# Kernel tuning notes

Hardware: AMD Instinct MI355X
Metric: run time of the kernel (lower is better)

The kernel has to match this reference:

```python
import jax, jax.numpy as jnp
import numpy as np

NUM_USERS = 50000
NUM_ITEMS = 40000
EMB = 64
NNZ = 2_000_000
BATCH = 1024


def setup_inputs() -> dict:
    key = jax.random.key(0)
    ks = jax.random.split(key, 10)
    graph_rows = jax.random.randint(ks[0], (NNZ,), 0, NUM_USERS, dtype=jnp.int32)
    graph_cols = jax.random.randint(ks[1], (NNZ,), 0, NUM_ITEMS, dtype=jnp.int32)
    graph_vals = jax.random.uniform(ks[2], (NNZ,), dtype=jnp.float32)
    Wq = jax.random.normal(ks[3], (2 * EMB, NUM_ITEMS), dtype=jnp.float32) * 0.01
    bq = jnp.zeros((2 * EMB,), jnp.float32)
    Wp = jax.random.normal(ks[4], (NUM_ITEMS, EMB), dtype=jnp.float32) * 0.01
    bp = jnp.zeros((NUM_ITEMS,), jnp.float32)
    user = jax.random.randint(ks[5], (BATCH,), 0, NUM_USERS, dtype=jnp.int32)
    x = (jax.random.uniform(ks[6], (BATCH, NUM_ITEMS)) < 0.02).astype(jnp.float32)
    eps = jax.random.normal(ks[7], (NUM_USERS, EMB), dtype=jnp.float32)
    return dict(graph_vals=graph_vals, Wq=Wq, bq=bq, Wp=Wp, bp=bp, x=x,
                eps=eps, graph_rows=graph_rows, graph_cols=graph_cols, user=user)


def reference(graph_vals, Wq, bq, Wp, bp, x, eps, graph_rows, graph_cols, user):
    # ---- encode: single SpMM  h = Graph @ Wq^T + bq   (dropout off / eval mode)
    # gather item rows of Wq^T per nonzero, scale, scatter-add into users
    gathered = graph_vals[:, None] * Wq.T[graph_cols]          # [nnz, 2E]
    h = jax.ops.segment_sum(gathered, graph_rows, num_segments=NUM_USERS) + bq  # [U, 2E]
    mu, logvar = h[:, :EMB], h[:, EMB:]                        # [U, E] each
    # ---- reparameterize: z = mu + eps * exp(0.5*logvar)
    z = mu + eps * jnp.exp(0.5 * logvar)
    # ---- decode batch users: single Linear(E -> I)
    zb = z[user]                                               # [B, E]
    recon = zb @ Wp.T + bp                                     # [B, I]
    # ---- Mult-VAE ELBO (anneal = 1.0)
    log_sm = jax.nn.log_softmax(recon, axis=-1)
    recon_loss = -jnp.mean(jnp.sum(log_sm * x, axis=-1))
    mu_b, lv_b = mu[user], logvar[user]
    kl_loss = -0.5 * jnp.mean(jnp.sum(1.0 + lv_b - mu_b * mu_b - jnp.exp(lv_b), axis=-1))
    return jnp.stack([recon_loss, kl_loss])  # [2]: (recon_loss, KL_loss)
```

## Files before the change

### kernel.cpp

```cpp
#include <hip/hip_runtime.h>
#include <cstdint>

#define NUM_USERS 50000
#define NUM_ITEMS 40000
#define EMB 64
#define NNZ_E 2000000
#define BATCH 1024
#define NCHB 125
#define SLOT_CAP 128
#define INF_I 0x7fffffff

typedef __attribute__((ext_vector_type(8))) short short8;
typedef __attribute__((ext_vector_type(4))) float float4v;

__device__ __forceinline__ unsigned short f2bf(float f) {
    union { float f; unsigned u; } x; x.f = f;
    unsigned r = x.u + 0x7fffu + ((x.u >> 16) & 1u);
    return (unsigned short)(r >> 16);
}
__device__ __forceinline__ float bf2f(unsigned short s) {
    return __uint_as_float(((unsigned)s) << 16);
}

__global__ __launch_bounds__(256) void k_init(int* __restrict__ map, int* __restrict__ cnt,
                                              float* __restrict__ scal, int2* __restrict__ compact) {
    int t = blockIdx.x * blockDim.x + threadIdx.x;
    if (t < NUM_USERS) map[t] = INF_I;
    if (t < BATCH) cnt[t] = 0;
    if (t < 4) scal[t] = 0.f;
    if (t < BATCH * SLOT_CAP) compact[t] = make_int2(0, 0);
}

__global__ void k_map(const int* __restrict__ user, int* __restrict__ map) {
    int i = blockIdx.x * blockDim.x + threadIdx.x;
    if (i < BATCH) atomicMin(&map[user[i]], i);
}

__global__ __launch_bounds__(256) void k_prep(const float* __restrict__ Wq,
                                              const float* __restrict__ Wp,
                                              unsigned short* __restrict__ WqT,
                                              unsigned short* __restrict__ WpBf) {
    __shared__ float t[128][33];
    const int bid = blockIdx.x;
    const int tid = threadIdx.x;
    if (bid < 1250) {
        const int jb = bid * 32;
        for (int idx = tid; idx < 4096; idx += 256) {
            int d = idx >> 5, c = idx & 31;
            t[d][c] = Wq[(size_t)d * NUM_ITEMS + jb + c];
        }
        __syncthreads();
        for (int idx = tid; idx < 4096; idx += 256) {
            int j = idx >> 7, d = idx & 127;
            WqT[(size_t)(jb + j) * 128 + d] = f2bf(t[d][j]);
        }
    } else {
        const int e0 = ((bid - 1250) * 256 + tid) * 4;
        float4 w = *(const float4*)&Wp[e0];
        ushort4 o;
        o.x = f2bf(w.x); o.y = f2bf(w.y); o.z = f2bf(w.z); o.w = f2bf(w.w);
        *(ushort4*)&WpBf[e0] = o;
    }
}

__global__ __launch_bounds__(256) void k_scatter(const int* __restrict__ rows,
                                                 const int* __restrict__ cols,
                                                 const float* __restrict__ vals,
                                                 const int* __restrict__ map,
                                                 int* __restrict__ cnt,
                                                 int2* __restrict__ compact) {
    const int e = blockIdx.x * 256 + threadIdx.x;
    if (e >= NNZ_E) return;
    int s = map[rows[e]];
    if (s == INF_I) return;
    int pos = atomicAdd(&cnt[s], 1);
    if (pos < SLOT_CAP) compact[s * SLOT_CAP + pos] = make_int2(cols[e], __float_as_int(vals[e]));
}

__global__ __launch_bounds__(128) void k_hz(const int* __restrict__ user,
                                            const int* __restrict__ map,
                                            const int* __restrict__ cnt,
                                            const int2* __restrict__ compact,
                                            const unsigned short* __restrict__ WqT,
                                            const float* __restrict__ bq,
                                            const float* __restrict__ eps,
                                            unsigned short* __restrict__ zbBf,
                                            float* __restrict__ scal) {
    __shared__ float sh[128];
    const int i = blockIdx.x;
    const int tid = threadIdx.x;
    const int u = user[i];
    const int s = map[u];
    const int n4 = (min(cnt[s], SLOT_CAP) + 3) & ~3;
    const int2* cp = compact + s * SLOT_CAP;
    float acc = 0.f;
    for (int e = 0; e < n4; e += 4) {
        int2 c0 = cp[e], c1 = cp[e + 1], c2 = cp[e + 2], c3 = cp[e + 3];
        float w0 = bf2f(WqT[(size_t)c0.x * 128 + tid]);
        float w1 = bf2f(WqT[(size_t)c1.x * 128 + tid]);
        float w2 = bf2f(WqT[(size_t)c2.x * 128 + tid]);
        float w3 = bf2f(WqT[(size_t)c3.x * 128 + tid]);
        acc = fmaf(__int_as_float(c0.y), w0, acc);
        acc = fmaf(__int_as_float(c1.y), w1, acc);
        acc = fmaf(__int_as_float(c2.y), w2, acc);
        acc = fmaf(__int_as_float(c3.y), w3, acc);
    }
    sh[tid] = acc + bq[tid];
    __syncthreads();
    if (tid < 64) {
        float mu = sh[tid];
        float lv = sh[tid + 64];
        float z = mu + eps[(size_t)u * EMB + tid] * __expf(0.5f * lv);
        zbBf[i * EMB + tid] = f2bf(z);
        float kl = 1.0f + lv - mu * mu - __expf(lv);
        #pragma unroll
        for (int o = 32; o; o >>= 1) kl += __shfl_down(kl, o);
        if (tid == 0) atomicAdd(&scal[1], kl);
    }
}

__global__ __launch_bounds__(256) void k_gemm(const unsigned short* __restrict__ zbBf,
                                              const unsigned short* __restrict__ WpBf,
                                              const float* __restrict__ bp,
                                              const float* __restrict__ x,
                                              float4* __restrict__ part) {
    const int tid = threadIdx.x;
    const int wid = tid >> 6, lane = tid & 63;
    const int l15 = lane & 15, quad = lane >> 4;
    const int ibase = blockIdx.y * 128 + wid * 32;

    short8 af[2][2];
    #pragma unroll
    for (int mt = 0; mt < 2; mt++) {
        const unsigned short* pa = zbBf + (size_t)(ibase + mt * 16 + l15) * EMB + quad * 8;
        af[mt][0] = *(const short8*)pa;
        af[mt][1] = *(const short8*)(pa + 32);
    }

    float m_run[2][4], s_run[2][4], dxa[2][4], sxa[2][4];
    #pragma unroll
    for (int mt = 0; mt < 2; mt++)
        #pragma unroll
        for (int r = 0; r < 4; r++) {
            m_run[mt][r] = -1e30f; s_run[mt][r] = 0.f;
            dxa[mt][r] = 0.f; sxa[mt][r] = 0.f;
        }

    #pragma unroll
    for (int c5 = 0; c5 < 5; c5++) {
        const int jb = blockIdx.x * 320 + c5 * 64;
        short8 bfr[4][2];
        #pragma unroll
        for (int nt = 0; nt < 4; nt++) {
            const unsigned short* pb = WpBf + (size_t)(jb + nt * 16 + l15) * EMB + quad * 8;
            bfr[nt][0] = *(const short8*)pb;
            bfr[nt][1] = *(const short8*)(pb + 32);
        }
        float4v acc[2][4];
        #pragma unroll
        for (int mt = 0; mt < 2; mt++)
            #pragma unroll
            for (int nt = 0; nt < 4; nt++)
                acc[mt][nt] = (float4v){0.f, 0.f, 0.f, 0.f};
        #pragma unroll
        for (int kh = 0; kh < 2; kh++)
            #pragma unroll
            for (int mt = 0; mt < 2; mt++)
                #pragma unroll
                for (int nt = 0; nt < 4; nt++)
                    acc[mt][nt] = __builtin_amdgcn_mfma_f32_16x16x32_bf16(
                        af[mt][kh], bfr[nt][kh], acc[mt][nt], 0, 0, 0);
        float bpv[4];
        #pragma unroll
        for (int nt = 0; nt < 4; nt++) bpv[nt] = bp[jb + nt * 16 + l15];
        #pragma unroll
        for (int mt = 0; mt < 2; mt++) {
            #pragma unroll
            for (int r = 0; r < 4; r++) {
                const float* xp = x + (size_t)(ibase + mt * 16 + quad * 4 + r) * NUM_ITEMS
                                    + jb + l15;
                float x0 = xp[0], x1 = xp[16], x2 = xp[32], x3 = xp[48];
                float v0 = acc[mt][0][r] + bpv[0];
                float v1 = acc[mt][1][r] + bpv[1];
                float v2 = acc[mt][2][r] + bpv[2];
                float v3 = acc[mt][3][r] + bpv[3];
                float mx = fmaxf(fmaxf(v0, v1), fmaxf(v2, v3));
                float M2 = fmaxf(m_run[mt][r], mx);
                float ls = __expf(v0 - M2) + __expf(v1 - M2) +
                           __expf(v2 - M2) + __expf(v3 - M2);
                s_run[mt][r] = s_run[mt][r] * __expf(m_run[mt][r] - M2) + ls;
                m_run[mt][r] = M2;
                dxa[mt][r] += v0 * x0 + v1 * x1 + v2 * x2 + v3 * x3;
                sxa[mt][r] += x0 + x1 + x2 + x3;
            }
        }
    }
    #pragma unroll
    for (int d = 1; d < 16; d <<= 1) {
        #pragma unroll
        for (int mt = 0; mt < 2; mt++)
            #pragma unroll
            for (int r = 0; r < 4; r++) {
                float m2 = __shfl_xor(m_run[mt][r], d);
                float s2 = __shfl_xor(s_run[mt][r], d);
                float M = fmaxf(m_run[mt][r], m2);
                s_run[mt][r] = s_run[mt][r] * __expf(m_run[mt][r] - M)
                             + s2 * __expf(m2 - M);
                m_run[mt][r] = M;
                dxa[mt][r] += __shfl_xor(dxa[mt][r], d);
                sxa[mt][r] += __shfl_xor(sxa[mt][r], d);
            }
    }
    if (l15 == 0) {
        #pragma unroll
        for (int mt = 0; mt < 2; mt++)
            #pragma unroll
            for (int r = 0; r < 4; r++) {
                const int gi = ibase + mt * 16 + quad * 4 + r;
                part[(size_t)gi * NCHB + blockIdx.x] =
                    make_float4(m_run[mt][r], s_run[mt][r], dxa[mt][r], sxa[mt][r]);
            }
    }
}

__global__ __launch_bounds__(64) void k_merge(const float4* __restrict__ part,
                                              float* __restrict__ scal) {
    const int row = blockIdx.x;
    const int lane = threadIdx.x;
    float M = -1e30f, S = 0.f, DX = 0.f, SX = 0.f;
    for (int c = lane; c < NCHB; c += 64) {
        float4 p = part[(size_t)row * NCHB + c];
        float M2 = fmaxf(M, p.x);
        S = S * __expf(M - M2) + p.y * __expf(p.x - M2);
        M = M2; DX += p.z; SX += p.w;
    }
    #pragma unroll
    for (int d = 1; d < 64; d <<= 1) {
        float M2 = __shfl_xor(M, d);
        float S2 = __shfl_xor(S, d);
        float DX2 = __shfl_xor(DX, d);
        float SX2 = __shfl_xor(SX, d);
        float Mn = fmaxf(M, M2);
        S = S * __expf(M - Mn) + S2 * __expf(M2 - Mn);
        M = Mn; DX += DX2; SX += SX2;
    }
    if (lane == 0) {
        float lse = M + logf(S);
        float loss = DX - lse * SX;
        atomicAdd(&scal[0], loss);
    }
}

__global__ void k_final(const float* __restrict__ scal, float* __restrict__ out) {
    if (threadIdx.x == 0 && blockIdx.x == 0) {
        out[0] = -scal[0] * (1.0f / BATCH);
        out[1] = -0.5f * scal[1] * (1.0f / BATCH);
    }
}

extern "C" void kernel_launch(void* const* d_in, const int* in_sizes, int n_in,
                              void* d_out, int out_size, void* d_ws, size_t ws_size,
                              hipStream_t stream) {
    const float* graph_vals = (const float*)d_in[0];
    const float* Wq         = (const float*)d_in[1];
    const float* bq         = (const float*)d_in[2];
    const float* Wp         = (const float*)d_in[3];
    const float* bp         = (const float*)d_in[4];
    const float* x          = (const float*)d_in[5];
    const float* eps        = (const float*)d_in[6];
    const int*   graph_rows = (const int*)d_in[7];
    const int*   graph_cols = (const int*)d_in[8];
    const int*   user       = (const int*)d_in[9];
    float* out = (float*)d_out;

    char* ws = (char*)d_ws;
    int*            map     = (int*)(ws + 0);
    int*            cnt     = (int*)(ws + 200704);
    float*          scal    = (float*)(ws + 204800);
    int2*           compact = (int2*)(ws + 205056);
    unsigned short* zbBf    = (unsigned short*)(ws + 1253632);
    unsigned short* WpBf    = (unsigned short*)(ws + 1384704);
    unsigned short* WqT     = (unsigned short*)(ws + 6504704);
    float4*         part    = (float4*)(ws + 16744704);

    k_init<<<512, 256, 0, stream>>>(map, cnt, scal, compact);
    k_map<<<4, 256, 0, stream>>>(user, map);
    k_prep<<<3750, 256, 0, stream>>>(Wq, Wp, WqT, WpBf);
    k_scatter<<<7813, 256, 0, stream>>>(graph_rows, graph_cols, graph_vals, map, cnt, compact);
    k_hz<<<BATCH, 128, 0, stream>>>(user, map, cnt, compact, WqT, bq, eps, zbBf, scal);
    dim3 g(NCHB, BATCH / 128);
    k_gemm<<<g, 256, 0, stream>>>(zbBf, WpBf, bp, x, part);
    k_merge<<<BATCH, 64, 0, stream>>>(part, scal);
    k_final<<<1, 64, 0, stream>>>(scal, out);
}
```

Before: 349.2 us.

## Compute x·recon via sparse x@Wp projection instead of dense x reads in GEMM

Rewrites the dot product of x with the logits algebraically as z·(x Wp) + x·bp. A new kernel scans each x row, uses ballots to find nonzeros, and accumulates x-weighted Wp rows plus the sums of x and x·bp. The GEMM then computes only the softmax log-sum-exp and writes smaller partials, so its strided dense loads of x go away. k_hz is also widened to 256 threads that split the nonzeros across warps with paired loads. x is still read once, densely, in the new pass, and Wp is gathered in fp32 per nonzero.

```diff
diff --git a/kernel.cpp b/kernel.cpp
--- a/kernel.cpp
+++ b/kernel.cpp
@@ -77,7 +77,7 @@
     if (pos < SLOT_CAP) compact[s * SLOT_CAP + pos] = make_int2(cols[e], __float_as_int(vals[e]));
 }
 
-__global__ __launch_bounds__(128) void k_hz(const int* __restrict__ user,
+__global__ __launch_bounds__(256) void k_hz(const int* __restrict__ user,
                                             const int* __restrict__ map,
                                             const int* __restrict__ cnt,
                                             const int2* __restrict__ compact,
@@ -85,45 +85,93 @@
                                             const float* __restrict__ bq,
                                             const float* __restrict__ eps,
                                             unsigned short* __restrict__ zbBf,
+                                            float* __restrict__ zF32,
                                             float* __restrict__ scal) {
-    __shared__ float sh[128];
+    __shared__ float sh[4][128];
     const int i = blockIdx.x;
     const int tid = threadIdx.x;
+    const int w = tid >> 6, lane = tid & 63;
     const int u = user[i];
     const int s = map[u];
-    const int n4 = (min(cnt[s], SLOT_CAP) + 3) & ~3;
+    const int n8 = (min(cnt[s], SLOT_CAP) + 7) & ~7;
     const int2* cp = compact + s * SLOT_CAP;
-    float acc = 0.f;
-    for (int e = 0; e < n4; e += 4) {
-        int2 c0 = cp[e], c1 = cp[e + 1], c2 = cp[e + 2], c3 = cp[e + 3];
-        float w0 = bf2f(WqT[(size_t)c0.x * 128 + tid]);
-        float w1 = bf2f(WqT[(size_t)c1.x * 128 + tid]);
-        float w2 = bf2f(WqT[(size_t)c2.x * 128 + tid]);
-        float w3 = bf2f(WqT[(size_t)c3.x * 128 + tid]);
-        acc = fmaf(__int_as_float(c0.y), w0, acc);
-        acc = fmaf(__int_as_float(c1.y), w1, acc);
-        acc = fmaf(__int_as_float(c2.y), w2, acc);
-        acc = fmaf(__int_as_float(c3.y), w3, acc);
-    }
-    sh[tid] = acc + bq[tid];
+    float ax = 0.f, ay = 0.f;
+    for (int e = w; e < n8; e += 8) {
+        int2 c0 = cp[e], c1 = cp[e + 4];
+        ushort2 w0 = *(const ushort2*)&WqT[(size_t)c0.x * 128 + lane * 2];
+        ushort2 w1 = *(const ushort2*)&WqT[(size_t)c1.x * 128 + lane * 2];
+        float v0 = __int_as_float(c0.y), v1 = __int_as_float(c1.y);
+        ax = fmaf(v0, bf2f(w0.x), ax);
+        ay = fmaf(v0, bf2f(w0.y), ay);
+        ax = fmaf(v1, bf2f(w1.x), ax);
+        ay = fmaf(v1, bf2f(w1.y), ay);
+    }
+    sh[w][lane * 2] = ax;
+    sh[w][lane * 2 + 1] = ay;
+    __syncthreads();
+    float h = 0.f;
+    if (tid < 128) h = sh[0][tid] + sh[1][tid] + sh[2][tid] + sh[3][tid] + bq[tid];
+    __syncthreads();
+    if (tid < 128) sh[0][tid] = h;
     __syncthreads();
     if (tid < 64) {
-        float mu = sh[tid];
-        float lv = sh[tid + 64];
-        float z = mu + eps[(size_t)u * EMB + tid] * __expf(0.5f * lv);
+        float mu = sh[0][tid];
+        float lv = sh[0][tid + 64];
+        float z = fmaf(eps[(size_t)u * EMB + tid], __expf(0.5f * lv), mu);
         zbBf[i * EMB + tid] = f2bf(z);
+        zF32[i * EMB + tid] = z;
         float kl = 1.0f + lv - mu * mu - __expf(lv);
         #pragma unroll
         for (int o = 32; o; o >>= 1) kl += __shfl_down(kl, o);
         if (tid == 0) atomicAdd(&scal[1], kl);
     }
+}
+
+__global__ __launch_bounds__(256) void k_xpass(const float* __restrict__ x,
+                                               const float* __restrict__ Wp,
+                                               const float* __restrict__ bp,
+                                               float* __restrict__ xWp,
+                                               float2* __restrict__ rowAux) {
+    __shared__ float sacc[4][EMB];
+    __shared__ float sscal[4][2];
+    const int row = blockIdx.x;
+    const int tid = threadIdx.x;
+    const int w = tid >> 6, lane = tid & 63;
+    const float4* xr = (const float4*)(x + (size_t)row * NUM_ITEMS);
+    float acc = 0.f, sx = 0.f, xb = 0.f;
+    for (int k = 0; k < 40; k++) {
+        const int idx4 = k * 256 + (w << 6) + lane;
+        float4 xv = make_float4(0.f, 0.f, 0.f, 0.f);
+        if (idx4 < 10000) xv = xr[idx4];
+        #pragma unroll
+        for (int q = 0; q < 4; q++) {
+            float v = (q == 0) ? xv.x : (q == 1) ? xv.y : (q == 2) ? xv.z : xv.w;
+            unsigned long long b = __ballot(v != 0.f);
+            while (b) {
+                const int sbit = __ffsll((long long)b) - 1;
+                b &= b - 1;
+                const float xs = __shfl(v, sbit);
+                const int j = ((k * 256 + (w << 6) + sbit) << 2) + q;
+                acc = fmaf(xs, Wp[(size_t)j * EMB + lane], acc);
+                sx += xs;
+                xb = fmaf(xs, bp[j], xb);
+            }
+        }
+    }
+    sacc[w][lane] = acc;
+    if (lane == 0) { sscal[w][0] = sx; sscal[w][1] = xb; }
+    __syncthreads();
+    if (tid < EMB)
+        xWp[(size_t)row * EMB + tid] = sacc[0][tid] + sacc[1][tid] + sacc[2][tid] + sacc[3][tid];
+    if (tid == 0)
+        rowAux[row] = make_float2(sscal[0][0] + sscal[1][0] + sscal[2][0] + sscal[3][0],
+                                  sscal[0][1] + sscal[1][1] + sscal[2][1] + sscal[3][1]);
 }
 
 __global__ __launch_bounds__(256) void k_gemm(const unsigned short* __restrict__ zbBf,
                                               const unsigned short* __restrict__ WpBf,
                                               const float* __restrict__ bp,
-                                              const float* __restrict__ x,
-                                              float4* __restrict__ part) {
+                                              float2* __restrict__ part) {
     const int tid = threadIdx.x;
     const int wid = tid >> 6, lane = tid & 63;
     const int l15 = lane & 15, quad = lane >> 4;
@@ -137,14 +185,11 @@
         af[mt][1] = *(const short8*)(pa + 32);
     }
 
-    float m_run[2][4], s_run[2][4], dxa[2][4], sxa[2][4];
+    float m_run[2][4], s_run[2][4];
     #pragma unroll
     for (int mt = 0; mt < 2; mt++)
         #pragma unroll
-        for (int r = 0; r < 4; r++) {
-            m_run[mt][r] = -1e30f; s_run[mt][r] = 0.f;
-            dxa[mt][r] = 0.f; sxa[mt][r] = 0.f;
-        }
+        for (int r = 0; r < 4; r++) { m_run[mt][r] = -1e30f; s_run[mt][r] = 0.f; }
 
     #pragma unroll
     for (int c5 = 0; c5 < 5; c5++) {
@@ -177,9 +222,6 @@
         for (int mt = 0; mt < 2; mt++) {
             #pragma unroll
             for (int r = 0; r < 4; r++) {
-                const float* xp = x + (size_t)(ibase + mt * 16 + quad * 4 + r) * NUM_ITEMS
-                                    + jb + l15;
-                float x0 = xp[0], x1 = xp[16], x2 = xp[32], x3 = xp[48];
                 float v0 = acc[mt][0][r] + bpv[0];
                 float v1 = acc[mt][1][r] + bpv[1];
                 float v2 = acc[mt][2][r] + bpv[2];
@@ -190,8 +232,6 @@
                            __expf(v2 - M2) + __expf(v3 - M2);
                 s_run[mt][r] = s_run[mt][r] * __expf(m_run[mt][r] - M2) + ls;
                 m_run[mt][r] = M2;
-                dxa[mt][r] += v0 * x0 + v1 * x1 + v2 * x2 + v3 * x3;
-                sxa[mt][r] += x0 + x1 + x2 + x3;
             }
         }
     }
@@ -207,8 +247,6 @@
                 s_run[mt][r] = s_run[mt][r] * __expf(m_run[mt][r] - M)
                              + s2 * __expf(m2 - M);
                 m_run[mt][r] = M;
-                dxa[mt][r] += __shfl_xor(dxa[mt][r], d);
-                sxa[mt][r] += __shfl_xor(sxa[mt][r], d);
             }
     }
     if (l15 == 0) {
@@ -218,35 +256,39 @@
             for (int r = 0; r < 4; r++) {
                 const int gi = ibase + mt * 16 + quad * 4 + r;
                 part[(size_t)gi * NCHB + blockIdx.x] =
-                    make_float4(m_run[mt][r], s_run[mt][r], dxa[mt][r], sxa[mt][r]);
+                    make_float2(m_run[mt][r], s_run[mt][r]);
             }
     }
 }
 
-__global__ __launch_bounds__(64) void k_merge(const float4* __restrict__ part,
+__global__ __launch_bounds__(64) void k_merge(const float2* __restrict__ part,
+                                              const float* __restrict__ zF32,
+                                              const float* __restrict__ xWp,
+                                              const float2* __restrict__ rowAux,
                                               float* __restrict__ scal) {
     const int row = blockIdx.x;
     const int lane = threadIdx.x;
-    float M = -1e30f, S = 0.f, DX = 0.f, SX = 0.f;
+    float M = -1e30f, S = 0.f;
     for (int c = lane; c < NCHB; c += 64) {
-        float4 p = part[(size_t)row * NCHB + c];
+        float2 p = part[(size_t)row * NCHB + c];
         float M2 = fmaxf(M, p.x);
         S = S * __expf(M - M2) + p.y * __expf(p.x - M2);
-        M = M2; DX += p.z; SX += p.w;
-    }
-    #pragma unroll
-    for (int d = 1; d < 64; d <<= 1) {
-        float M2 = __shfl_xor(M, d);
-        float S2 = __shfl_xor(S, d);
-        float DX2 = __shfl_xor(DX, d);
-        float SX2 = __shfl_xor(SX, d);
+        M = M2;
+    }
+    float d = zF32[(size_t)row * EMB + lane] * xWp[(size_t)row * EMB + lane];
+    #pragma unroll
+    for (int o = 1; o < 64; o <<= 1) {
+        float M2 = __shfl_xor(M, o);
+        float S2 = __shfl_xor(S, o);
         float Mn = fmaxf(M, M2);
         S = S * __expf(M - Mn) + S2 * __expf(M2 - Mn);
-        M = Mn; DX += DX2; SX += SX2;
+        M = Mn;
+        d += __shfl_xor(d, o);
     }
     if (lane == 0) {
+        float2 aux = rowAux[row];
         float lse = M + logf(S);
-        float loss = DX - lse * SX;
+        float loss = d + aux.y - lse * aux.x;
         atomicAdd(&scal[0], loss);
     }
 }
@@ -279,17 +321,21 @@
     float*          scal    = (float*)(ws + 204800);
     int2*           compact = (int2*)(ws + 205056);
     unsigned short* zbBf    = (unsigned short*)(ws + 1253632);
-    unsigned short* WpBf    = (unsigned short*)(ws + 1384704);
-    unsigned short* WqT     = (unsigned short*)(ws + 6504704);
-    float4*         part    = (float4*)(ws + 16744704);
+    float*          zF32    = (float*)(ws + 1384704);
+    float*          xWp     = (float*)(ws + 1646848);
+    float2*         rowAux  = (float2*)(ws + 1908992);
+    float2*         part    = (float2*)(ws + 1917184);
+    unsigned short* WpBf    = (unsigned short*)(ws + 2941184);
+    unsigned short* WqT     = (unsigned short*)(ws + 8061184);
 
     k_init<<<512, 256, 0, stream>>>(map, cnt, scal, compact);
     k_map<<<4, 256, 0, stream>>>(user, map);
     k_prep<<<3750, 256, 0, stream>>>(Wq, Wp, WqT, WpBf);
     k_scatter<<<7813, 256, 0, stream>>>(graph_rows, graph_cols, graph_vals, map, cnt, compact);
-    k_hz<<<BATCH, 128, 0, stream>>>(user, map, cnt, compact, WqT, bq, eps, zbBf, scal);
+    k_hz<<<BATCH, 256, 0, stream>>>(user, map, cnt, compact, WqT, bq, eps, zbBf, zF32, scal);
+    k_xpass<<<BATCH, 256, 0, stream>>>(x, Wp, bp, xWp, rowAux);
     dim3 g(NCHB, BATCH / 128);
-    k_gemm<<<g, 256, 0, stream>>>(zbBf, WpBf, bp, x, part);
-    k_merge<<<BATCH, 64, 0, stream>>>(part, scal);
+    k_gemm<<<g, 256, 0, stream>>>(zbBf, WpBf, bp, part);
+    k_merge<<<BATCH, 64, 0, stream>>>(part, zF32, xWp, rowAux, scal);
     k_final<<<1, 64, 0, stream>>>(scal, out);
 }
```

New measurement: 450.0 us. 1.29x slower.
